# Kernel optimization log

Measured on AMD Instinct MI355X. Metric: run time of the kernel, lower is better.

The kernel has to match this reference:

```python
import jax, jax.numpy as jnp
import numpy as np

HIDDEN = 2048
INPUT = 2048
BATCH = 4096


def setup_inputs() -> dict:
    key = jax.random.key(0)
    ks = jax.random.split(key, 7)
    x = jax.random.normal(ks[0], (BATCH, INPUT), dtype=jnp.float32)
    h = jax.random.normal(ks[1], (BATCH, HIDDEN), dtype=jnp.float32)
    c = jax.random.normal(ks[2], (BATCH, HIDDEN), dtype=jnp.float32)
    # learned parameters (RandomNormal init stddev=0.05 analogue; scale irrelevant for correctness)
    w_ih = jax.random.normal(ks[3], (4, INPUT, HIDDEN), dtype=jnp.float32) * 0.05
    w_hh = jax.random.normal(ks[4], (4, HIDDEN, HIDDEN), dtype=jnp.float32) * 0.05
    b_ih = jax.random.normal(ks[5], (4, HIDDEN), dtype=jnp.float32) * 0.05
    b_hh = jax.random.normal(ks[6], (4, HIDDEN), dtype=jnp.float32) * 0.05
    return {"x": x, "h": h, "c": c, "w_ih": w_ih, "w_hh": w_hh, "b_ih": b_ih, "b_hh": b_hh}


def reference(x, h, c, w_ih, w_hh, b_ih, b_hh):
    # gates: [4, B, H] = x @ w_ih[g] and h @ w_hh[g], batched over gate dim g
    gates = (
        jnp.einsum("bi,gih->gbh", x, w_ih)
        + jnp.einsum("bh,ghk->gbk", h, w_hh)
        + (b_ih + b_hh)[:, None, :]
    )
    ingate = jax.nn.sigmoid(gates[0])
    forgetgate = jax.nn.sigmoid(gates[1])
    cellgate = jnp.tanh(gates[2])
    outgate = jax.nn.sigmoid(gates[3])
    c_new = forgetgate * c + ingate * cellgate
    h_new = outgate * jnp.tanh(c_new)
    return (h_new, c_new)
```

## Files before the change

kernel.cpp:

```cpp
#include <hip/hip_runtime.h>

#define BATCH  4096
#define HIDDEN 2048
#define INPUT  2048
#define KDIM   4096
#define NDIM   8192
#define BM 128
#define BN 128
#define BK 32

typedef __attribute__((ext_vector_type(8))) short short8;
typedef __attribute__((ext_vector_type(4))) float float4v;


__device__ __forceinline__ unsigned short f2bf(float f) {
    union { float f; unsigned u; } v; v.f = f;
    unsigned r = v.u + 0x7FFFu + ((v.u >> 16) & 1u);
    return (unsigned short)(r >> 16);
}

__device__ __forceinline__ void gl2lds16(const unsigned short* g, unsigned short* l) {
    __builtin_amdgcn_global_load_lds(
        (const __attribute__((address_space(1))) unsigned int*)g,
        (__attribute__((address_space(3))) unsigned int*)l,
        16, 0, 0);
}

__device__ __forceinline__ float sigm(float x) {
    return 1.0f / (1.0f + __expf(-x));
}
__device__ __forceinline__ float tanh_fast(float x) {
    return 2.0f / (1.0f + __expf(-2.0f * x)) - 1.0f;
}


__global__ void pack_x_kernel(const float* __restrict__ x, const float* __restrict__ h,
                              unsigned short* __restrict__ Xb) {
    int idx = blockIdx.x * 256 + threadIdx.x;
    int b  = idx >> 9;
    int ko = idx & 511;
    const float* src = (ko < 256) ? (x + (size_t)b * INPUT  + (size_t)ko * 8)
                                  : (h + (size_t)b * HIDDEN + (size_t)(ko - 256) * 8);
    float4 v0 = *(const float4*)(src);
    float4 v1 = *(const float4*)(src + 4);
    union { unsigned short us[8]; uint4 v; } o;
    o.us[0] = f2bf(v0.x); o.us[1] = f2bf(v0.y); o.us[2] = f2bf(v0.z); o.us[3] = f2bf(v0.w);
    o.us[4] = f2bf(v1.x); o.us[5] = f2bf(v1.y); o.us[6] = f2bf(v1.z); o.us[7] = f2bf(v1.w);
    *(uint4*)(Xb + (size_t)b * KDIM + (size_t)ko * 8) = o.v;
}


__global__ void pack_w_kernel(const float* __restrict__ w_ih, const float* __restrict__ w_hh,
                              unsigned short* __restrict__ Wt) {
    __shared__ float tile[64][33];
    int k0 = blockIdx.x * 64;
    int n0 = blockIdx.y * 32;
    int g  = n0 >> 11;
    int j0 = n0 & 2047;
    const float* src = (k0 < INPUT)
        ? (w_ih + (size_t)g * INPUT  * HIDDEN + (size_t)k0 * HIDDEN + j0)
        : (w_hh + (size_t)g * HIDDEN * HIDDEN + (size_t)(k0 - INPUT) * HIDDEN + j0);

    int tcol = threadIdx.x & 31;
    int trow = threadIdx.x >> 5;
#pragma unroll
    for (int p = 0; p < 8; ++p)
        tile[trow + p * 8][tcol] = src[(size_t)(trow + p * 8) * HIDDEN + tcol];
    __syncthreads();

    int tk = threadIdx.x & 63;
    int tn = threadIdx.x >> 6;
#pragma unroll
    for (int p = 0; p < 8; ++p) {
        int j = j0 + tn + p * 4;
        Wt[(size_t)(4 * j + g) * KDIM + k0 + tk] = f2bf(tile[tk][tn + p * 4]);
    }
}


__global__ __launch_bounds__(256, 2)
void gemm_kernel(const unsigned short* __restrict__ A,
                 const unsigned short* __restrict__ B,
                 const float* __restrict__ c,
                 const float* __restrict__ b_ih,
                 const float* __restrict__ b_hh,
                 float* __restrict__ out) {
    __shared__ unsigned short As[BM * BK];
    __shared__ unsigned short Bs[BN * BK];

    const int tid  = threadIdx.x;
    const int m0   = blockIdx.y * BM;
    const int n0   = blockIdx.x * BN;
    const int wave = tid >> 6;
    const int lane = tid & 63;
    const int ln   = lane & 15;
    const int kq   = lane >> 4;
    const int wm   = (wave >> 1) * 64;
    const int wn   = (wave & 1) * 64;

    const int s0 = tid, s1 = tid + 256;
    const unsigned short* gA0 = A + (size_t)(m0 + (s0 >> 2)) * KDIM + (s0 & 3) * 8;
    const unsigned short* gA1 = A + (size_t)(m0 + (s1 >> 2)) * KDIM + (s1 & 3) * 8;
    const unsigned short* gB0 = B + (size_t)(n0 + (s0 >> 2)) * KDIM + (s0 & 3) * 8;
    const unsigned short* gB1 = B + (size_t)(n0 + (s1 >> 2)) * KDIM + (s1 & 3) * 8;
    unsigned short* lA0 = As + s0 * 8;
    unsigned short* lA1 = As + s1 * 8;
    unsigned short* lB0 = Bs + s0 * 8;
    unsigned short* lB1 = Bs + s1 * 8;

    float4v acc[4][4];
#pragma unroll
    for (int i = 0; i < 4; ++i)
#pragma unroll
        for (int j = 0; j < 4; ++j)
            acc[i][j] = (float4v){0.f, 0.f, 0.f, 0.f};

    const int a_off = (wm + ln) * BK + kq * 8;
    const int b_off = (wn + ln) * BK + kq * 8;

    for (int kt = 0; kt < KDIM / BK; ++kt) {
        const int ko = kt * BK;
        gl2lds16(gA0 + ko, lA0);
        gl2lds16(gA1 + ko, lA1);
        gl2lds16(gB0 + ko, lB0);
        gl2lds16(gB1 + ko, lB1);
        __syncthreads();

        short8 af[4], bfr[4];
#pragma unroll
        for (int mi = 0; mi < 4; ++mi)
            af[mi] = *(const short8*)(As + a_off + mi * 16 * BK);
#pragma unroll
        for (int ni = 0; ni < 4; ++ni)
            bfr[ni] = *(const short8*)(Bs + b_off + ni * 16 * BK);

#pragma unroll
        for (int mi = 0; mi < 4; ++mi)
#pragma unroll
            for (int ni = 0; ni < 4; ++ni)
                acc[mi][ni] = __builtin_amdgcn_mfma_f32_16x16x32_bf16(
                    af[mi], bfr[ni], acc[mi][ni], 0, 0, 0);

        __syncthreads();
    }

    const int q = lane & 3;
    const int t = (lane & 15) >> 2;
    const size_t HB = (size_t)BATCH * HIDDEN;

#pragma unroll
    for (int ni = 0; ni < 4; ++ni) {
        const int jg = ((n0 + wn + ni * 16) >> 2) + t;
        const float b0 = b_ih[jg]              + b_hh[jg];
        const float b1 = b_ih[HIDDEN + jg]     + b_hh[HIDDEN + jg];
        const float b2 = b_ih[2 * HIDDEN + jg] + b_hh[2 * HIDDEN + jg];
        const float b3 = b_ih[3 * HIDDEN + jg] + b_hh[3 * HIDDEN + jg];
#pragma unroll
        for (int mi = 0; mi < 4; ++mi) {
            float4v v = acc[mi][ni];
            float t1 = __shfl_xor((q & 1) ? v[0] : v[1], 1);
            float t2 = __shfl_xor((q & 1) ? v[2] : v[3], 1);
            v[0] = (q & 1) ? t1 : v[0];
            v[1] = (q & 1) ? v[1] : t1;
            v[2] = (q & 1) ? t2 : v[2];
            v[3] = (q & 1) ? v[3] : t2;
            float t3 = __shfl_xor((q & 2) ? v[0] : v[2], 2);
            float t4 = __shfl_xor((q & 2) ? v[1] : v[3], 2);
            v[0] = (q & 2) ? t3 : v[0];
            v[1] = (q & 2) ? t4 : v[1];
            v[2] = (q & 2) ? v[2] : t3;
            v[3] = (q & 2) ? v[3] : t4;

            const int row = m0 + wm + mi * 16 + kq * 4 + q;
            const float ig = sigm(v[0] + b0);
            const float fg = sigm(v[1] + b1);
            const float cg = tanh_fast(v[2] + b2);
            const float og = sigm(v[3] + b3);
            const float cv = c[(size_t)row * HIDDEN + jg];
            const float cn = fg * cv + ig * cg;
            const float hn = og * tanh_fast(cn);
            out[(size_t)row * HIDDEN + jg] = hn;
            out[HB + (size_t)row * HIDDEN + jg] = cn;
        }
    }
}


extern "C" void kernel_launch(void* const* d_in, const int* in_sizes, int n_in,
                              void* d_out, int out_size, void* d_ws, size_t ws_size,
                              hipStream_t stream) {
    const float* x    = (const float*)d_in[0];
    const float* h    = (const float*)d_in[1];
    const float* c    = (const float*)d_in[2];
    const float* w_ih = (const float*)d_in[3];
    const float* w_hh = (const float*)d_in[4];
    const float* b_ih = (const float*)d_in[5];
    const float* b_hh = (const float*)d_in[6];
    float* out = (float*)d_out;

    const size_t XB_BYTES = (size_t)BATCH * KDIM * 2;
    unsigned short* Xb = (unsigned short*)d_ws;
    unsigned short* Wt = (unsigned short*)((char*)d_ws + XB_BYTES);

    hipLaunchKernelGGL(pack_x_kernel, dim3((size_t)BATCH * KDIM / 8 / 256), dim3(256), 0, stream,
                       x, h, Xb);
    hipLaunchKernelGGL(pack_w_kernel, dim3(KDIM / 64, NDIM / 32), dim3(256), 0, stream,
                       w_ih, w_hh, Wt);
    hipLaunchKernelGGL(gemm_kernel, dim3(NDIM / BN, BATCH / BM), dim3(256), 0, stream,
                       Xb, Wt, c, b_ih, b_hh, out);
}
```

Measured before the change: 565.0 us.

## Merge pack kernels and stage LSTM epilogue through LDS for coalesced stores

Merges the two pack kernels into one launch, with a block-index branch choosing between x/h packing and weight packing. In the GEMM, the c values and bias sums are loaded before the K loop, so their latency can overlap the main loop. The epilogue writes h and c tiles into reused LDS and then stores them to global memory with coalesced float4 writes, replacing the scattered 4-byte stores. This costs extra registers for the prefetched values, which may reduce occupancy, plus an extra barrier and LDS round-trip.

```diff
diff --git a/kernel.cpp b/kernel.cpp
--- a/kernel.cpp
+++ b/kernel.cpp
@@ -8,6 +8,7 @@
 #define BM 128
 #define BN 128
 #define BK 32
+#define EPI_STRIDE 36
 
 typedef __attribute__((ext_vector_type(8))) short short8;
 typedef __attribute__((ext_vector_type(4))) float float4v;
@@ -34,46 +35,47 @@
 }
 
 
-__global__ void pack_x_kernel(const float* __restrict__ x, const float* __restrict__ h,
-                              unsigned short* __restrict__ Xb) {
-    int idx = blockIdx.x * 256 + threadIdx.x;
-    int b  = idx >> 9;
-    int ko = idx & 511;
-    const float* src = (ko < 256) ? (x + (size_t)b * INPUT  + (size_t)ko * 8)
-                                  : (h + (size_t)b * HIDDEN + (size_t)(ko - 256) * 8);
-    float4 v0 = *(const float4*)(src);
-    float4 v1 = *(const float4*)(src + 4);
-    union { unsigned short us[8]; uint4 v; } o;
-    o.us[0] = f2bf(v0.x); o.us[1] = f2bf(v0.y); o.us[2] = f2bf(v0.z); o.us[3] = f2bf(v0.w);
-    o.us[4] = f2bf(v1.x); o.us[5] = f2bf(v1.y); o.us[6] = f2bf(v1.z); o.us[7] = f2bf(v1.w);
-    *(uint4*)(Xb + (size_t)b * KDIM + (size_t)ko * 8) = o.v;
-}
-
-
-__global__ void pack_w_kernel(const float* __restrict__ w_ih, const float* __restrict__ w_hh,
-                              unsigned short* __restrict__ Wt) {
+__global__ void pack_kernel(const float* __restrict__ x, const float* __restrict__ h,
+                            const float* __restrict__ w_ih, const float* __restrict__ w_hh,
+                            unsigned short* __restrict__ Xb, unsigned short* __restrict__ Wt) {
     __shared__ float tile[64][33];
-    int k0 = blockIdx.x * 64;
-    int n0 = blockIdx.y * 32;
-    int g  = n0 >> 11;
-    int j0 = n0 & 2047;
-    const float* src = (k0 < INPUT)
-        ? (w_ih + (size_t)g * INPUT  * HIDDEN + (size_t)k0 * HIDDEN + j0)
-        : (w_hh + (size_t)g * HIDDEN * HIDDEN + (size_t)(k0 - INPUT) * HIDDEN + j0);
-
-    int tcol = threadIdx.x & 31;
-    int trow = threadIdx.x >> 5;
-#pragma unroll
-    for (int p = 0; p < 8; ++p)
-        tile[trow + p * 8][tcol] = src[(size_t)(trow + p * 8) * HIDDEN + tcol];
-    __syncthreads();
-
-    int tk = threadIdx.x & 63;
-    int tn = threadIdx.x >> 6;
-#pragma unroll
-    for (int p = 0; p < 8; ++p) {
-        int j = j0 + tn + p * 4;
-        Wt[(size_t)(4 * j + g) * KDIM + k0 + tk] = f2bf(tile[tk][tn + p * 4]);
+    int bid = blockIdx.x;
+    if (bid < 8192) {
+        int idx = bid * 256 + threadIdx.x;
+        int b  = idx >> 9;
+        int ko = idx & 511;
+        const float* src = (ko < 256) ? (x + (size_t)b * INPUT  + (size_t)ko * 8)
+                                      : (h + (size_t)b * HIDDEN + (size_t)(ko - 256) * 8);
+        float4 v0 = *(const float4*)(src);
+        float4 v1 = *(const float4*)(src + 4);
+        union { unsigned short us[8]; uint4 v; } o;
+        o.us[0] = f2bf(v0.x); o.us[1] = f2bf(v0.y); o.us[2] = f2bf(v0.z); o.us[3] = f2bf(v0.w);
+        o.us[4] = f2bf(v1.x); o.us[5] = f2bf(v1.y); o.us[6] = f2bf(v1.z); o.us[7] = f2bf(v1.w);
+        *(uint4*)(Xb + (size_t)b * KDIM + (size_t)ko * 8) = o.v;
+    } else {
+        int wb = bid - 8192;
+        int k0 = (wb & 63) * 64;
+        int n0 = (wb >> 6) * 32;
+        int g  = n0 >> 11;
+        int j0 = n0 & 2047;
+        const float* src = (k0 < INPUT)
+            ? (w_ih + (size_t)g * INPUT  * HIDDEN + (size_t)k0 * HIDDEN + j0)
+            : (w_hh + (size_t)g * HIDDEN * HIDDEN + (size_t)(k0 - INPUT) * HIDDEN + j0);
+
+        int tcol = threadIdx.x & 31;
+        int trow = threadIdx.x >> 5;
+#pragma unroll
+        for (int p = 0; p < 8; ++p)
+            tile[trow + p * 8][tcol] = src[(size_t)(trow + p * 8) * HIDDEN + tcol];
+        __syncthreads();
+
+        int tk = threadIdx.x & 63;
+        int tn = threadIdx.x >> 6;
+#pragma unroll
+        for (int p = 0; p < 8; ++p) {
+            int j = j0 + tn + p * 4;
+            Wt[(size_t)(4 * j + g) * KDIM + k0 + tk] = f2bf(tile[tk][tn + p * 4]);
+        }
     }
 }
 
@@ -85,18 +87,24 @@
                  const float* __restrict__ b_ih,
                  const float* __restrict__ b_hh,
                  float* __restrict__ out) {
-    __shared__ unsigned short As[BM * BK];
-    __shared__ unsigned short Bs[BN * BK];
+    __shared__ __align__(16) char smem[2 * 128 * EPI_STRIDE * 4];
+    unsigned short* As = (unsigned short*)smem;
+    unsigned short* Bs = (unsigned short*)(smem + 8192);
+    float* hT = (float*)smem;
+    float* cT = (float*)(smem + 128 * EPI_STRIDE * 4);
 
     const int tid  = threadIdx.x;
     const int m0   = blockIdx.y * BM;
     const int n0   = blockIdx.x * BN;
+    const int jg0  = n0 >> 2;
     const int wave = tid >> 6;
     const int lane = tid & 63;
     const int ln   = lane & 15;
     const int kq   = lane >> 4;
     const int wm   = (wave >> 1) * 64;
     const int wn   = (wave & 1) * 64;
+    const int q    = lane & 3;
+    const int t    = (lane & 15) >> 2;
 
     const int s0 = tid, s1 = tid + 256;
     const unsigned short* gA0 = A + (size_t)(m0 + (s0 >> 2)) * KDIM + (s0 & 3) * 8;
@@ -115,6 +123,23 @@
         for (int j = 0; j < 4; ++j)
             acc[i][j] = (float4v){0.f, 0.f, 0.f, 0.f};
 
+    float cv[4][4];
+    float bsum[4][4];
+#pragma unroll
+    for (int mi = 0; mi < 4; ++mi) {
+        const int row = m0 + wm + mi * 16 + kq * 4 + q;
+#pragma unroll
+        for (int ni = 0; ni < 4; ++ni)
+            cv[mi][ni] = c[(size_t)row * HIDDEN + jg0 + (wn >> 2) + ni * 4 + t];
+    }
+#pragma unroll
+    for (int ni = 0; ni < 4; ++ni) {
+        const int jg = jg0 + (wn >> 2) + ni * 4 + t;
+#pragma unroll
+        for (int g = 0; g < 4; ++g)
+            bsum[ni][g] = b_ih[g * HIDDEN + jg] + b_hh[g * HIDDEN + jg];
+    }
+
     const int a_off = (wm + ln) * BK + kq * 8;
     const int b_off = (wn + ln) * BK + kq * 8;
 
@@ -144,17 +169,9 @@
         __syncthreads();
     }
 
-    const int q = lane & 3;
-    const int t = (lane & 15) >> 2;
-    const size_t HB = (size_t)BATCH * HIDDEN;
-
 #pragma unroll
     for (int ni = 0; ni < 4; ++ni) {
-        const int jg = ((n0 + wn + ni * 16) >> 2) + t;
-        const float b0 = b_ih[jg]              + b_hh[jg];
-        const float b1 = b_ih[HIDDEN + jg]     + b_hh[HIDDEN + jg];
-        const float b2 = b_ih[2 * HIDDEN + jg] + b_hh[2 * HIDDEN + jg];
-        const float b3 = b_ih[3 * HIDDEN + jg] + b_hh[3 * HIDDEN + jg];
+        const int jgL = (wn >> 2) + ni * 4 + t;
 #pragma unroll
         for (int mi = 0; mi < 4; ++mi) {
             float4v v = acc[mi][ni];
@@ -171,17 +188,30 @@
             v[2] = (q & 2) ? v[2] : t3;
             v[3] = (q & 2) ? v[3] : t4;
 
-            const int row = m0 + wm + mi * 16 + kq * 4 + q;
-            const float ig = sigm(v[0] + b0);
-            const float fg = sigm(v[1] + b1);
-            const float cg = tanh_fast(v[2] + b2);
-            const float og = sigm(v[3] + b3);
-            const float cv = c[(size_t)row * HIDDEN + jg];
-            const float cn = fg * cv + ig * cg;
+            const int rowL = wm + mi * 16 + kq * 4 + q;
+            const float ig = sigm(v[0] + bsum[ni][0]);
+            const float fg = sigm(v[1] + bsum[ni][1]);
+            const float cg = tanh_fast(v[2] + bsum[ni][2]);
+            const float og = sigm(v[3] + bsum[ni][3]);
+            const float cn = fg * cv[mi][ni] + ig * cg;
             const float hn = og * tanh_fast(cn);
-            out[(size_t)row * HIDDEN + jg] = hn;
-            out[HB + (size_t)row * HIDDEN + jg] = cn;
+            hT[rowL * EPI_STRIDE + jgL] = hn;
+            cT[rowL * EPI_STRIDE + jgL] = cn;
         }
+    }
+    __syncthreads();
+
+    const size_t HB = (size_t)BATCH * HIDDEN;
+#pragma unroll
+    for (int p = 0; p < 4; ++p) {
+        const int s   = tid + p * 256;
+        const int row = s >> 3;
+        const int c4  = s & 7;
+        float4 hv = *(const float4*)(hT + row * EPI_STRIDE + c4 * 4);
+        float4 cw = *(const float4*)(cT + row * EPI_STRIDE + c4 * 4);
+        const size_t go = (size_t)(m0 + row) * HIDDEN + jg0 + c4 * 4;
+        *(float4*)(out + go)      = hv;
+        *(float4*)(out + HB + go) = cw;
     }
 }
 
@@ -202,10 +232,8 @@
     unsigned short* Xb = (unsigned short*)d_ws;
     unsigned short* Wt = (unsigned short*)((char*)d_ws + XB_BYTES);
 
-    hipLaunchKernelGGL(pack_x_kernel, dim3((size_t)BATCH * KDIM / 8 / 256), dim3(256), 0, stream,
-                       x, h, Xb);
-    hipLaunchKernelGGL(pack_w_kernel, dim3(KDIM / 64, NDIM / 32), dim3(256), 0, stream,
-                       w_ih, w_hh, Wt);
+    hipLaunchKernelGGL(pack_kernel, dim3(8192 + 16384), dim3(256), 0, stream,
+                       x, h, w_ih, w_hh, Xb, Wt);
     hipLaunchKernelGGL(gemm_kernel, dim3(NDIM / BN, BATCH / BM), dim3(256), 0, stream,
                        Xb, Wt, c, b_ih, b_hh, out);
 }
```

Measured after the change: 571.8 us. No clear change (+1.2%).
